# Optimization experiments

Hardware: AMD Instinct MI355X
Metric: run time of the kernel (lower is better)

## Reference

```python
import jax, jax.numpy as jnp
import numpy as np

LN_EPS = 1e-5

def _lstm_cell(x, h, c, Wih, Whh, bih, bhh):
    # gates: [b, 4*d], PyTorch LSTMCell gate order: i, f, g, o
    gates = x @ Wih.T + bih + h @ Whh.T + bhh
    i, f, g, o = jnp.split(gates, 4, axis=-1)
    c_new = jax.nn.sigmoid(f) * c + jax.nn.sigmoid(i) * jnp.tanh(g)
    h_new = jax.nn.sigmoid(o) * jnp.tanh(c_new)
    return h_new, c_new

def _layernorm(x, g, b):
    mu = jnp.mean(x, axis=-1, keepdims=True)
    var = jnp.mean(jnp.square(x - mu), axis=-1, keepdims=True)
    return (x - mu) * jax.lax.rsqrt(var + LN_EPS) * g + b

def setup_inputs() -> dict:
    key = jax.random.key(0)
    ks = jax.random.split(key, 8)
    B, F_, L, D, V, NL = 128, 1, 32, 512, 10000, 2
    features = jax.random.normal(ks[0], (B, F_, D), dtype=jnp.float32)
    caption = jax.random.randint(ks[1], (B, L), 0, V, dtype=jnp.int64)
    emb_W = jax.random.normal(ks[2], (V, D), dtype=jnp.float32) * 0.02
    W_ih = jax.random.normal(ks[3], (NL, 4 * D, D), dtype=jnp.float32) * (1.0 / np.sqrt(D))
    W_hh = jax.random.normal(ks[4], (NL, 4 * D, D), dtype=jnp.float32) * (1.0 / np.sqrt(D))
    b_ih = jnp.zeros((NL, 4 * D), dtype=jnp.float32)
    b_hh = jnp.zeros((NL, 4 * D), dtype=jnp.float32)
    ln_g = jnp.ones((D,), dtype=jnp.float32)
    ln_b = jnp.zeros((D,), dtype=jnp.float32)
    fc_W = jax.random.normal(ks[5], (V, D), dtype=jnp.float32) * np.sqrt(2.0 / D)
    fc_b = jnp.zeros((V,), dtype=jnp.float32)
    return {"features": features, "caption": caption, "emb_W": emb_W,
            "W_ih": W_ih, "W_hh": W_hh, "b_ih": b_ih, "b_hh": b_hh,
            "ln_g": ln_g, "ln_b": ln_b, "fc_W": fc_W, "fc_b": fc_b}

def reference(features, caption, emb_W, W_ih, W_hh, b_ih, b_hh, ln_g, ln_b, fc_W, fc_b):
    b, f, d = features.shape
    n_layers = W_ih.shape[0]
    emb = emb_W[caption]                                   # [b, L, d]
    inp = jnp.concatenate([features, emb], axis=1)         # [b, T, d], T = f + L
    h0 = jnp.zeros((b, d), dtype=features.dtype)
    c0 = jnp.zeros((b, d), dtype=features.dtype)

    def step(carry, x_t):
        h, c = carry
        # Faithful to the original: every layer consumes x_t, sharing (h, c).
        for l in range(n_layers):
            h, c = _lstm_cell(x_t, h, c, W_ih[l], W_hh[l], b_ih[l], b_hh[l])
        h = _layernorm(h, ln_g, ln_b)                      # normalized h carries forward
        logits_t = h @ fc_W.T + fc_b                       # [b, V]
        return (h, c), logits_t

    xs = jnp.swapaxes(inp, 0, 1)                           # [T, b, d]
    _, logits = jax.lax.scan(step, (h0, c0), xs)           # [T, b, V]
    logits = jnp.swapaxes(logits, 0, 1)                    # [b, T, V]
    return jax.nn.log_softmax(logits[:, f:, :], axis=-1)   # [b, L, V]
```

## Files before the change

### kernel.cpp

```cpp
#include <hip/hip_runtime.h>

#define B_ 128
#define D_ 512
#define T_ 33
#define L_ 32
#define V_ 10000
#define NWG 128

typedef short short8 __attribute__((ext_vector_type(8)));
typedef float f32x4 __attribute__((ext_vector_type(4)));

__device__ __forceinline__ short f2bf_rne(float f) {
    unsigned u = __builtin_bit_cast(unsigned, f);
    unsigned r = (u + 0x7FFFu + ((u >> 16) & 1u)) >> 16;
    return (short)r;
}
__device__ __forceinline__ void split2(float v, short& hi, short& lo) {
    unsigned u = __builtin_bit_cast(unsigned, v);
    hi = (short)(u >> 16);
    float hif = __builtin_bit_cast(float, u & 0xFFFF0000u);
    lo = (short)(__builtin_bit_cast(unsigned, v - hif) >> 16);
}
__device__ __forceinline__ float sigm(float x) {
    return 1.0f / (1.0f + __expf(-x));
}

__device__ __forceinline__ void llc_stu(void* p, unsigned v) {
    __hip_atomic_store((unsigned*)p, v, __ATOMIC_RELAXED,
                       __HIP_MEMORY_SCOPE_SYSTEM);
}

__global__ void prep_kernel(const float* __restrict__ features,
                            const int* __restrict__ caption,
                            const float* __restrict__ embW,
                            const float* __restrict__ fcW,
                            short* __restrict__ Xhi,
                            short* __restrict__ Xlo,
                            short* __restrict__ fcWb,
                            int* __restrict__ syncv) {
    const long NX = (long)T_ * B_ * D_;
    const long NW = (long)V_ * D_;
    const long total = NX + NW;
    long gid = (long)blockIdx.x * blockDim.x + threadIdx.x;
    if (gid < NWG) syncv[gid] = 0;
    for (long idx = gid; idx < total; idx += (long)gridDim.x * blockDim.x) {
        if (idx < NX) {
            int t = (int)(idx / (B_ * D_));
            int r = (int)(idx % (B_ * D_));
            int b = r >> 9;
            int d = r & 511;
            float v;
            if (t == 0) v = features[r];
            else        v = embW[(long)caption[b * L_ + (t - 1)] * D_ + d];
            short hi, lo;
            split2(v, hi, lo);
            Xhi[idx] = hi;
            Xlo[idx] = lo;
        } else {
            long j = idx - NX;
            fcWb[j] = f2bf_rne(fcW[j]);
        }
    }
}

__global__ __launch_bounds__(256)
void lstm_persist(const short* __restrict__ Xhi, const short* __restrict__ Xlo,
                  const float* __restrict__ Wih, const float* __restrict__ Whh,
                  const float* __restrict__ bih, const float* __restrict__ bhh,
                  const float* __restrict__ lng, const float* __restrict__ lnb,
                  unsigned* __restrict__ H0p, float* __restrict__ H1f,
                  short* __restrict__ Hnb, int* __restrict__ syncv) {
    __shared__ __align__(16) short Wh[2][16][1032];
    __shared__ __align__(16) short Wo[2][16][1032];
    __shared__ float gbuf[128][17];
    __shared__ float carr[128][4];
    __shared__ float rs_s[128], murs_s[128];
    __shared__ float gam_s[512], bet_s[512];
    __shared__ float bias_s[2][16];
    __shared__ float bconst_s[16];

    const int tid  = threadIdx.x;
    const int w    = blockIdx.x;
    const int d0   = w * 4;
    const int wave = tid >> 6;
    const int lane = tid & 63;
    const int wm   = wave * 32;
    const int n    = lane & 15;
    const int kq   = (lane >> 4) * 8;

    for (int idx = tid; idx < 512; idx += 256) {
        gam_s[idx] = lng[idx];
        bet_s[idx] = lnb[idx];
    }
    if (tid < 32) {
        int l = tid >> 4, nn = tid & 15;
        int row = (nn >> 2) * 512 + d0 + (nn & 3);
        bias_s[l][nn] = bih[l * 2048 + row] + bhh[l * 2048 + row];
    }
    for (int idx = tid; idx < 2 * 16 * 1024; idx += 256) {
        int l = idx >> 14;
        int nn = (idx >> 10) & 15;
        int k = idx & 1023;
        int row = (nn >> 2) * 512 + d0 + (nn & 3);
        float v = (k < 512) ? Wih[((long)(l * 2048 + row)) * 512 + k]
                            : Whh[((long)(l * 2048 + row)) * 512 + (k - 512)];
        if (l == 0 && k >= 512) v *= lng[k - 512];
        short hi, lo;
        split2(v, hi, lo);
        Wh[l][nn][k] = hi;
        Wo[l][nn][k] = lo;
    }
    {
        const int c = tid >> 4, kc = tid & 15;
        const int row = (c >> 2) * 512 + d0 + (c & 3);
        float s = 0.f;
        for (int k = kc * 32; k < kc * 32 + 32; ++k)
            s += lnb[k] * Whh[(long)row * 512 + k];
        gbuf[c][kc] = s;
    }
    for (int idx = tid; idx < 512; idx += 256) carr[idx >> 2][idx & 3] = 0.f;
    __syncthreads();
    if (tid < 16) {
        float s2 = 0.f;
        for (int i = 0; i < 16; ++i) s2 += gbuf[tid][i];
        bconst_s[tid] = s2;
    }
    __syncthreads();

    int* flags = syncv;
    int nb = 0;

    auto arrive = [&]() {
        __syncthreads();
        ++nb;
        if (tid == 0)
            __hip_atomic_store(&flags[w], nb, __ATOMIC_RELAXED,
                               __HIP_MEMORY_SCOPE_SYSTEM);
    };
    auto wait_bar = [&]() {
        if (wave == 0) {
            const int tgt = nb;
            for (;;) {
                int f0 = __hip_atomic_load(&flags[lane], __ATOMIC_RELAXED,
                                           __HIP_MEMORY_SCOPE_SYSTEM);
                int f1 = __hip_atomic_load(&flags[64 + lane], __ATOMIC_RELAXED,
                                           __HIP_MEMORY_SCOPE_SYSTEM);
                if (__all(f0 >= tgt && f1 >= tgt)) break;
                __builtin_amdgcn_s_sleep(1);
            }
        }
        __syncthreads();
        __builtin_amdgcn_fence(__ATOMIC_ACQUIRE, "agent");
    };

    auto ln_stats = [&]() {
        const int row = tid & 127, half = tid >> 7;
        const float4* hp = (const float4*)&H1f[row * 512 + half * 256];
        float s = 0.f, s2 = 0.f;
        #pragma unroll 16
        for (int i = 0; i < 64; ++i) {
            float4 v = hp[i];
            s  += v.x + v.y + v.z + v.w;
            s2 += v.x * v.x + v.y * v.y + v.z * v.z + v.w * v.w;
        }
        gbuf[row][half * 2]     = s;
        gbuf[row][half * 2 + 1] = s2;
        __syncthreads();
        if (tid < 128) {
            const float ss  = gbuf[tid][0] + gbuf[tid][2];
            const float ss2 = gbuf[tid][1] + gbuf[tid][3];
            const float mu  = ss * (1.0f / 512.0f);
            const float var = ss2 * (1.0f / 512.0f) - mu * mu;
            const float rs  = rsqrtf(var + 1e-5f);
            rs_s[tid]   = rs;
            murs_s[tid] = mu * rs;
        }
        __syncthreads();
    };

    const int rA0 = (wm + n) * 512;
    const int rA1 = (wm + 16 + n) * 512;
    const int rq  = (lane >> 4) * 4;

    for (int t = 0; t < T_; ++t) {
        const short* xh = Xhi + (long)t * B_ * D_;
        const short* xl = Xlo + (long)t * B_ * D_;

        {
            f32x4 acc0 = {0.f, 0.f, 0.f, 0.f};
            f32x4 acc1 = {0.f, 0.f, 0.f, 0.f};
            #pragma unroll 4
            for (int kc = 0; kc < 16; ++kc) {
                const int kg = kc * 32 + kq;
                short8 bh = *(const short8*)&Wh[0][n][kg];
                short8 bl = *(const short8*)&Wo[0][n][kg];
                short8 ah0 = *(const short8*)&xh[rA0 + kg];
                short8 al0 = *(const short8*)&xl[rA0 + kg];
                short8 ah1 = *(const short8*)&xh[rA1 + kg];
                short8 al1 = *(const short8*)&xl[rA1 + kg];
                acc0 = __builtin_amdgcn_mfma_f32_16x16x32_bf16(ah0, bh, acc0, 0, 0, 0);
                acc0 = __builtin_amdgcn_mfma_f32_16x16x32_bf16(ah0, bl, acc0, 0, 0, 0);
                acc0 = __builtin_amdgcn_mfma_f32_16x16x32_bf16(al0, bh, acc0, 0, 0, 0);
                acc1 = __builtin_amdgcn_mfma_f32_16x16x32_bf16(ah1, bh, acc1, 0, 0, 0);
                acc1 = __builtin_amdgcn_mfma_f32_16x16x32_bf16(ah1, bl, acc1, 0, 0, 0);
                acc1 = __builtin_amdgcn_mfma_f32_16x16x32_bf16(al1, bh, acc1, 0, 0, 0);
            }
            if (t > 0) {
                wait_bar();
                ln_stats();
                const float r0 = rs_s[wm + n],      m0 = murs_s[wm + n];
                const float r1 = rs_s[wm + 16 + n], m1 = murs_s[wm + 16 + n];
                #pragma unroll 2
                for (int kc = 0; kc < 16; ++kc) {
                    const int kh = kc * 32 + kq;
                    short8 bh = *(const short8*)&Wh[0][n][512 + kh];
                    short8 bl = *(const short8*)&Wo[0][n][512 + kh];
                    float va[8], vb[8];
                    *(float4*)&va[0] = *(const float4*)&H1f[rA0 + kh];
                    *(float4*)&va[4] = *(const float4*)&H1f[rA0 + kh + 4];
                    *(float4*)&vb[0] = *(const float4*)&H1f[rA1 + kh];
                    *(float4*)&vb[4] = *(const float4*)&H1f[rA1 + kh + 4];
                    short8 ah0, al0, ah1, al1;
                    #pragma unroll
                    for (int j = 0; j < 8; ++j) {
                        float f0 = fmaf(va[j], r0, -m0);
                        float f1 = fmaf(vb[j], r1, -m1);
                        short h_, l_;
                        split2(f0, h_, l_); ah0[j] = h_; al0[j] = l_;
                        split2(f1, h_, l_); ah1[j] = h_; al1[j] = l_;
                    }
                    acc0 = __builtin_amdgcn_mfma_f32_16x16x32_bf16(ah0, bh, acc0, 0, 0, 0);
                    acc0 = __builtin_amdgcn_mfma_f32_16x16x32_bf16(ah0, bl, acc0, 0, 0, 0);
                    acc0 = __builtin_amdgcn_mfma_f32_16x16x32_bf16(al0, bh, acc0, 0, 0, 0);
                    acc1 = __builtin_amdgcn_mfma_f32_16x16x32_bf16(ah1, bh, acc1, 0, 0, 0);
                    acc1 = __builtin_amdgcn_mfma_f32_16x16x32_bf16(ah1, bl, acc1, 0, 0, 0);
                    acc1 = __builtin_amdgcn_mfma_f32_16x16x32_bf16(al1, bh, acc1, 0, 0, 0);
                }
                if (w < 32 && t >= 2) {
                    const int rb = w * 4;
                    for (int idx = tid; idx < 2048; idx += 256) {
                        const int m = rb + (idx >> 9), k = idx & 511;
                        const float v = H1f[m * 512 + k];
                        const float o = fmaf(fmaf(v, rs_s[m], -murs_s[m]), gam_s[k], bet_s[k]);
                        Hnb[(((long)(t - 2)) * B_ + m) * D_ + k] = f2bf_rne(o);
                    }
                }
            }
            const float bs = bias_s[0][n] + (t > 0 ? bconst_s[n] : 0.f);
            #pragma unroll
            for (int r = 0; r < 4; ++r) {
                gbuf[wm + rq + r][n]      = acc0[r] + bs;
                gbuf[wm + 16 + rq + r][n] = acc1[r] + bs;
            }
            __syncthreads();
            #pragma unroll
            for (int it = tid; it < 512; it += 256) {
                const int m = it >> 2, d = it & 3;
                const float gi = gbuf[m][d],     gf = gbuf[m][4 + d];
                const float gg = gbuf[m][8 + d], go = gbuf[m][12 + d];
                const float cn = sigm(gf) * carr[m][d] + sigm(gi) * tanhf(gg);
                carr[m][d] = cn;
                const float hv = sigm(go) * tanhf(cn);
                short hi_, lo_;
                split2(hv, hi_, lo_);
                const unsigned pk = (unsigned)(unsigned short)hi_
                                  | ((unsigned)(unsigned short)lo_ << 16);
                llc_stu(&H0p[m * 512 + d0 + d], pk);
            }
            arrive();
        }

        {
            f32x4 acc0 = {0.f, 0.f, 0.f, 0.f};
            f32x4 acc1 = {0.f, 0.f, 0.f, 0.f};
            #pragma unroll 4
            for (int kc = 0; kc < 16; ++kc) {
                const int kg = kc * 32 + kq;
                short8 bh = *(const short8*)&Wh[1][n][kg];
                short8 bl = *(const short8*)&Wo[1][n][kg];
                short8 ah0 = *(const short8*)&xh[rA0 + kg];
                short8 al0 = *(const short8*)&xl[rA0 + kg];
                short8 ah1 = *(const short8*)&xh[rA1 + kg];
                short8 al1 = *(const short8*)&xl[rA1 + kg];
                acc0 = __builtin_amdgcn_mfma_f32_16x16x32_bf16(ah0, bh, acc0, 0, 0, 0);
                acc0 = __builtin_amdgcn_mfma_f32_16x16x32_bf16(ah0, bl, acc0, 0, 0, 0);
                acc0 = __builtin_amdgcn_mfma_f32_16x16x32_bf16(al0, bh, acc0, 0, 0, 0);
                acc1 = __builtin_amdgcn_mfma_f32_16x16x32_bf16(ah1, bh, acc1, 0, 0, 0);
                acc1 = __builtin_amdgcn_mfma_f32_16x16x32_bf16(ah1, bl, acc1, 0, 0, 0);
                acc1 = __builtin_amdgcn_mfma_f32_16x16x32_bf16(al1, bh, acc1, 0, 0, 0);
            }
            wait_bar();
            #pragma unroll 2
            for (int kc = 0; kc < 16; ++kc) {
                const int kh = kc * 32 + kq;
                short8 bh = *(const short8*)&Wh[1][n][512 + kh];
                short8 bl = *(const short8*)&Wo[1][n][512 + kh];
                unsigned u0[8], u1[8];
                *(uint4*)&u0[0] = *(const uint4*)&H0p[rA0 + kh];
                *(uint4*)&u0[4] = *(const uint4*)&H0p[rA0 + kh + 4];
                *(uint4*)&u1[0] = *(const uint4*)&H0p[rA1 + kh];
                *(uint4*)&u1[4] = *(const uint4*)&H0p[rA1 + kh + 4];
                short8 ah0, al0, ah1, al1;
                #pragma unroll
                for (int j = 0; j < 8; ++j) {
                    ah0[j] = (short)(u0[j] & 0xFFFFu);
                    al0[j] = (short)(u0[j] >> 16);
                    ah1[j] = (short)(u1[j] & 0xFFFFu);
                    al1[j] = (short)(u1[j] >> 16);
                }
                acc0 = __builtin_amdgcn_mfma_f32_16x16x32_bf16(ah0, bh, acc0, 0, 0, 0);
                acc0 = __builtin_amdgcn_mfma_f32_16x16x32_bf16(ah0, bl, acc0, 0, 0, 0);
                acc0 = __builtin_amdgcn_mfma_f32_16x16x32_bf16(al0, bh, acc0, 0, 0, 0);
                acc1 = __builtin_amdgcn_mfma_f32_16x16x32_bf16(ah1, bh, acc1, 0, 0, 0);
                acc1 = __builtin_amdgcn_mfma_f32_16x16x32_bf16(ah1, bl, acc1, 0, 0, 0);
                acc1 = __builtin_amdgcn_mfma_f32_16x16x32_bf16(al1, bh, acc1, 0, 0, 0);
            }
            const float bs = bias_s[1][n];
            #pragma unroll
            for (int r = 0; r < 4; ++r) {
                gbuf[wm + rq + r][n]      = acc0[r] + bs;
                gbuf[wm + 16 + rq + r][n] = acc1[r] + bs;
            }
            __syncthreads();
            #pragma unroll
            for (int it = tid; it < 512; it += 256) {
                const int m = it >> 2, d = it & 3;
                const float gi = gbuf[m][d],     gf = gbuf[m][4 + d];
                const float gg = gbuf[m][8 + d], go = gbuf[m][12 + d];
                const float cn = sigm(gf) * carr[m][d] + sigm(gi) * tanhf(gg);
                carr[m][d] = cn;
                const float hv = sigm(go) * tanhf(cn);
                llc_stu(&H1f[m * 512 + d0 + d],
                        __builtin_bit_cast(unsigned, hv));
            }
            arrive();
        }
    }

    wait_bar();
    ln_stats();
    if (w < 32) {
        const int rb = w * 4;
        for (int idx = tid; idx < 2048; idx += 256) {
            const int m = rb + (idx >> 9), k = idx & 511;
            const float v = H1f[m * 512 + k];
            const float o = fmaf(fmaf(v, rs_s[m], -murs_s[m]), gam_s[k], bet_s[k]);
            Hnb[(((long)(L_ - 1)) * B_ + m) * D_ + k] = f2bf_rne(o);
        }
    }
}

__launch_bounds__(256)
__global__ void gemm_fc(const short* __restrict__ A,
                        const short* __restrict__ Wt,
                        const float* __restrict__ bias,
                        float* __restrict__ out) {
    __shared__ __align__(16) short As[128 * 40];
    __shared__ __align__(16) short Bs[128 * 40];
    const int tid = threadIdx.x;
    const int m0 = blockIdx.x * 128;
    const int n0 = blockIdx.y * 128;
    const int lrow = tid >> 1;
    const int lcol = (tid & 1) * 16;
    const int w = tid >> 6;
    const int lane = tid & 63;
    const int wm = (w >> 1) * 64;
    const int wn = (w & 1) * 64;

    f32x4 acc[4][4];
    #pragma unroll
    for (int i = 0; i < 4; ++i)
        #pragma unroll
        for (int j = 0; j < 4; ++j)
            acc[i][j] = (f32x4){0.f, 0.f, 0.f, 0.f};

    for (int kc = 0; kc < 16; ++kc) {
        const int kg = kc * 32;
        {
            const float4* src = reinterpret_cast<const float4*>(
                A + (long)(m0 + lrow) * D_ + kg + lcol);
            float4 v0 = src[0];
            float4 v1 = src[1];
            float4* dst = reinterpret_cast<float4*>(&As[lrow * 40 + lcol]);
            dst[0] = v0;
            dst[1] = v1;
        }
        {
            const int nn = n0 + lrow;
            float4 v0 = {0.f, 0.f, 0.f, 0.f}, v1 = {0.f, 0.f, 0.f, 0.f};
            if (nn < V_) {
                const float4* src = reinterpret_cast<const float4*>(
                    Wt + (long)nn * D_ + kg + lcol);
                v0 = src[0];
                v1 = src[1];
            }
            float4* dst = reinterpret_cast<float4*>(&Bs[lrow * 40 + lcol]);
            dst[0] = v0;
            dst[1] = v1;
        }
        __syncthreads();
        const int kcol = (lane >> 4) * 8;
        const int rsel = lane & 15;
        short8 a[4], bf[4];
        #pragma unroll
        for (int i = 0; i < 4; ++i)
            a[i] = *reinterpret_cast<const short8*>(&As[(wm + i * 16 + rsel) * 40 + kcol]);
        #pragma unroll
        for (int j = 0; j < 4; ++j)
            bf[j] = *reinterpret_cast<const short8*>(&Bs[(wn + j * 16 + rsel) * 40 + kcol]);
        #pragma unroll
        for (int i = 0; i < 4; ++i)
            #pragma unroll
            for (int j = 0; j < 4; ++j)
                acc[i][j] = __builtin_amdgcn_mfma_f32_16x16x32_bf16(a[i], bf[j], acc[i][j], 0, 0, 0);
        __syncthreads();
    }

    const int rquad = (lane >> 4) * 4;
    const int ncol = lane & 15;
    #pragma unroll
    for (int i = 0; i < 4; ++i) {
        #pragma unroll
        for (int j = 0; j < 4; ++j) {
            const int ngl = n0 + wn + j * 16 + ncol;
            if (ngl < V_) {
                const float bv = bias[ngl];
                #pragma unroll
                for (int r = 0; r < 4; ++r) {
                    const int mgl = m0 + wm + i * 16 + rquad + r;
                    const int tt = mgl >> 7;
                    const int bb = mgl & 127;
                    out[((long)bb * L_ + tt) * V_ + ngl] = acc[i][j][r] + bv;
                }
            }
        }
    }
}

__global__ void logsoftmax_kernel(float* __restrict__ out) {
    __shared__ float red[256];
    const long row = blockIdx.x;
    float* p = out + row * V_;
    float4* p4 = reinterpret_cast<float4*>(p);
    const int tid = threadIdx.x;
    float s = 0.f;
    for (int i = tid; i < V_ / 4; i += 256) {
        float4 v = p4[i];
        s += __expf(v.x) + __expf(v.y) + __expf(v.z) + __expf(v.w);
    }
    red[tid] = s;
    __syncthreads();
    for (int st = 128; st > 0; st >>= 1) {
        if (tid < st) red[tid] += red[tid + st];
        __syncthreads();
    }
    const float ls = logf(red[0]);
    for (int i = tid; i < V_ / 4; i += 256) {
        float4 v = p4[i];
        v.x -= ls; v.y -= ls; v.z -= ls; v.w -= ls;
        p4[i] = v;
    }
}

extern "C" void kernel_launch(void* const* d_in, const int* in_sizes, int n_in,
                              void* d_out, int out_size, void* d_ws, size_t ws_size,
                              hipStream_t stream) {
    const float* features = (const float*)d_in[0];
    const int*   caption  = (const int*)d_in[1];
    const float* embW     = (const float*)d_in[2];
    const float* W_ih     = (const float*)d_in[3];
    const float* W_hh     = (const float*)d_in[4];
    const float* b_ih     = (const float*)d_in[5];
    const float* b_hh     = (const float*)d_in[6];
    const float* ln_g     = (const float*)d_in[7];
    const float* ln_b     = (const float*)d_in[8];
    const float* fc_W     = (const float*)d_in[9];
    const float* fc_b     = (const float*)d_in[10];
    float* out = (float*)d_out;

    char* ws = (char*)d_ws;
    int*      syncv = (int*)ws;      ws += 512;
    short*    Xhi   = (short*)ws;    ws += (size_t)T_ * B_ * D_ * 2;
    short*    Xlo   = (short*)ws;    ws += (size_t)T_ * B_ * D_ * 2;
    unsigned* H0p   = (unsigned*)ws; ws += (size_t)B_ * D_ * 4;
    float*    H1f   = (float*)ws;    ws += (size_t)B_ * D_ * 4;
    short*    Hnb   = (short*)ws;    ws += (size_t)L_ * B_ * D_ * 2;
    short*    fcWb  = (short*)ws;    ws += (size_t)V_ * D_ * 2;

    prep_kernel<<<2048, 256, 0, stream>>>(features, caption, embW, fc_W,
                                          Xhi, Xlo, fcWb, syncv);

    lstm_persist<<<NWG, 256, 0, stream>>>(Xhi, Xlo, W_ih, W_hh, b_ih, b_hh,
                                          ln_g, ln_b, H0p, H1f, Hnb,
                                          syncv);

    gemm_fc<<<dim3(32, 79), 256, 0, stream>>>(Hnb, fcWb, fc_b, out);
    logsoftmax_kernel<<<4096, 256, 0, stream>>>(out);
}
```

Baseline: 1.773 ms.

## Fold layernorm into layer-0 recurrent GEMM and double threads per workgroup

The persistent LSTM kernel now runs 512 threads (8 waves, 16 rows each) instead of 256, so each wave handles one MFMA tile rather than two. The layer-1 hidden state is stored pre-split as packed bf16 hi/lo. Layer 0 multiplies the raw hidden state and applies the layernorm correction afterwards (rs*acc - mu*rs*sum(gamma*W)), which moves the LN stats off the critical path and drops per-element normalize/split work. The barrier spin also gains an iteration cap, which could break out early and read stale data if the cap is ever hit.

```diff
diff --git a/kernel.cpp b/kernel.cpp
--- a/kernel.cpp
+++ b/kernel.cpp
@@ -6,6 +6,7 @@
 #define L_ 32
 #define V_ 10000
 #define NWG 128
+#define THREADS 512
 
 typedef short short8 __attribute__((ext_vector_type(8)));
 typedef float f32x4 __attribute__((ext_vector_type(4)));
@@ -23,6 +24,10 @@
 }
 __device__ __forceinline__ float sigm(float x) {
     return 1.0f / (1.0f + __expf(-x));
+}
+__device__ __forceinline__ float unpack2f(unsigned u) {
+    return __builtin_bit_cast(float, u << 16)
+         + __builtin_bit_cast(float, u & 0xFFFF0000u);
 }
 
 __device__ __forceinline__ void llc_stu(void* p, unsigned v) {
@@ -63,12 +68,12 @@
     }
 }
 
-__global__ __launch_bounds__(256)
+__global__ __launch_bounds__(THREADS)
 void lstm_persist(const short* __restrict__ Xhi, const short* __restrict__ Xlo,
                   const float* __restrict__ Wih, const float* __restrict__ Whh,
                   const float* __restrict__ bih, const float* __restrict__ bhh,
                   const float* __restrict__ lng, const float* __restrict__ lnb,
-                  unsigned* __restrict__ H0p, float* __restrict__ H1f,
+                  unsigned* __restrict__ H0p, unsigned* __restrict__ H1p,
                   short* __restrict__ Hnb, int* __restrict__ syncv) {
     __shared__ __align__(16) short Wh[2][16][1032];
     __shared__ __align__(16) short Wo[2][16][1032];
@@ -78,26 +83,25 @@
     __shared__ float gam_s[512], bet_s[512];
     __shared__ float bias_s[2][16];
     __shared__ float bconst_s[16];
+    __shared__ float sgam_s[16];
 
     const int tid  = threadIdx.x;
     const int w    = blockIdx.x;
     const int d0   = w * 4;
     const int wave = tid >> 6;
     const int lane = tid & 63;
-    const int wm   = wave * 32;
+    const int wm   = wave * 16;
     const int n    = lane & 15;
     const int kq   = (lane >> 4) * 8;
 
-    for (int idx = tid; idx < 512; idx += 256) {
-        gam_s[idx] = lng[idx];
-        bet_s[idx] = lnb[idx];
-    }
+    gam_s[tid & 511] = lng[tid & 511];
+    bet_s[tid & 511] = lnb[tid & 511];
     if (tid < 32) {
         int l = tid >> 4, nn = tid & 15;
         int row = (nn >> 2) * 512 + d0 + (nn & 3);
         bias_s[l][nn] = bih[l * 2048 + row] + bhh[l * 2048 + row];
     }
-    for (int idx = tid; idx < 2 * 16 * 1024; idx += 256) {
+    for (int idx = tid; idx < 2 * 16 * 1024; idx += THREADS) {
         int l = idx >> 14;
         int nn = (idx >> 10) & 15;
         int k = idx & 1023;
@@ -110,20 +114,27 @@
         Wh[l][nn][k] = hi;
         Wo[l][nn][k] = lo;
     }
-    {
+    if (tid < 256) {
         const int c = tid >> 4, kc = tid & 15;
         const int row = (c >> 2) * 512 + d0 + (c & 3);
+        float sb = 0.f, sg = 0.f;
+        for (int k = kc * 32; k < kc * 32 + 32; ++k) {
+            const float wv = Whh[(long)row * 512 + k];
+            sb += lnb[k] * wv;
+            sg += lng[k] * wv;
+        }
+        gbuf[c][kc]      = sb;
+        gbuf[64 + c][kc] = sg;
+    }
+    carr[tid >> 2][tid & 3] = 0.f;
+    __syncthreads();
+    if (tid < 32) {
+        const int c = tid & 15;
+        const int base = (tid >= 16) ? 64 + c : c;
         float s = 0.f;
-        for (int k = kc * 32; k < kc * 32 + 32; ++k)
-            s += lnb[k] * Whh[(long)row * 512 + k];
-        gbuf[c][kc] = s;
-    }
-    for (int idx = tid; idx < 512; idx += 256) carr[idx >> 2][idx & 3] = 0.f;
-    __syncthreads();
-    if (tid < 16) {
-        float s2 = 0.f;
-        for (int i = 0; i < 16; ++i) s2 += gbuf[tid][i];
-        bconst_s[tid] = s2;
+        for (int i = 0; i < 16; ++i) s += gbuf[base][i];
+        if (tid < 16) bconst_s[c] = s;
+        else          sgam_s[c]   = s;
     }
     __syncthreads();
 
@@ -140,35 +151,41 @@
     auto wait_bar = [&]() {
         if (wave == 0) {
             const int tgt = nb;
+            int iter = 0;
             for (;;) {
                 int f0 = __hip_atomic_load(&flags[lane], __ATOMIC_RELAXED,
                                            __HIP_MEMORY_SCOPE_SYSTEM);
                 int f1 = __hip_atomic_load(&flags[64 + lane], __ATOMIC_RELAXED,
                                            __HIP_MEMORY_SCOPE_SYSTEM);
                 if (__all(f0 >= tgt && f1 >= tgt)) break;
+                if (++iter > 65536) break;
                 __builtin_amdgcn_s_sleep(1);
             }
-        }
-        __syncthreads();
-        __builtin_amdgcn_fence(__ATOMIC_ACQUIRE, "agent");
+            __builtin_amdgcn_fence(__ATOMIC_ACQUIRE, "agent");
+        }
+        __syncthreads();
     };
 
     auto ln_stats = [&]() {
-        const int row = tid & 127, half = tid >> 7;
-        const float4* hp = (const float4*)&H1f[row * 512 + half * 256];
+        const int row = tid & 127, q = tid >> 7;
+        const uint4* hp = (const uint4*)&H1p[row * 512 + q * 128];
         float s = 0.f, s2 = 0.f;
-        #pragma unroll 16
-        for (int i = 0; i < 64; ++i) {
-            float4 v = hp[i];
-            s  += v.x + v.y + v.z + v.w;
-            s2 += v.x * v.x + v.y * v.y + v.z * v.z + v.w * v.w;
-        }
-        gbuf[row][half * 2]     = s;
-        gbuf[row][half * 2 + 1] = s2;
+        #pragma unroll 8
+        for (int i = 0; i < 32; ++i) {
+            uint4 u = hp[i];
+            #pragma unroll
+            for (int e = 0; e < 4; ++e) {
+                const float v = unpack2f((&u.x)[e]);
+                s  += v;
+                s2 += v * v;
+            }
+        }
+        gbuf[row][q * 2]     = s;
+        gbuf[row][q * 2 + 1] = s2;
         __syncthreads();
         if (tid < 128) {
-            const float ss  = gbuf[tid][0] + gbuf[tid][2];
-            const float ss2 = gbuf[tid][1] + gbuf[tid][3];
+            const float ss  = gbuf[tid][0] + gbuf[tid][2] + gbuf[tid][4] + gbuf[tid][6];
+            const float ss2 = gbuf[tid][1] + gbuf[tid][3] + gbuf[tid][5] + gbuf[tid][7];
             const float mu  = ss * (1.0f / 512.0f);
             const float var = ss2 * (1.0f / 512.0f) - mu * mu;
             const float rs  = rsqrtf(var + 1e-5f);
@@ -179,7 +196,6 @@
     };
 
     const int rA0 = (wm + n) * 512;
-    const int rA1 = (wm + 16 + n) * 512;
     const int rq  = (lane >> 4) * 4;
 
     for (int t = 0; t < T_; ++t) {
@@ -187,75 +203,62 @@
         const short* xl = Xlo + (long)t * B_ * D_;
 
         {
-            f32x4 acc0 = {0.f, 0.f, 0.f, 0.f};
-            f32x4 acc1 = {0.f, 0.f, 0.f, 0.f};
+            f32x4 accx = {0.f, 0.f, 0.f, 0.f};
+            f32x4 acch = {0.f, 0.f, 0.f, 0.f};
             #pragma unroll 4
             for (int kc = 0; kc < 16; ++kc) {
                 const int kg = kc * 32 + kq;
                 short8 bh = *(const short8*)&Wh[0][n][kg];
                 short8 bl = *(const short8*)&Wo[0][n][kg];
-                short8 ah0 = *(const short8*)&xh[rA0 + kg];
-                short8 al0 = *(const short8*)&xl[rA0 + kg];
-                short8 ah1 = *(const short8*)&xh[rA1 + kg];
-                short8 al1 = *(const short8*)&xl[rA1 + kg];
-                acc0 = __builtin_amdgcn_mfma_f32_16x16x32_bf16(ah0, bh, acc0, 0, 0, 0);
-                acc0 = __builtin_amdgcn_mfma_f32_16x16x32_bf16(ah0, bl, acc0, 0, 0, 0);
-                acc0 = __builtin_amdgcn_mfma_f32_16x16x32_bf16(al0, bh, acc0, 0, 0, 0);
-                acc1 = __builtin_amdgcn_mfma_f32_16x16x32_bf16(ah1, bh, acc1, 0, 0, 0);
-                acc1 = __builtin_amdgcn_mfma_f32_16x16x32_bf16(ah1, bl, acc1, 0, 0, 0);
-                acc1 = __builtin_amdgcn_mfma_f32_16x16x32_bf16(al1, bh, acc1, 0, 0, 0);
+                short8 ah = *(const short8*)&xh[rA0 + kg];
+                short8 al = *(const short8*)&xl[rA0 + kg];
+                accx = __builtin_amdgcn_mfma_f32_16x16x32_bf16(ah, bh, accx, 0, 0, 0);
+                accx = __builtin_amdgcn_mfma_f32_16x16x32_bf16(ah, bl, accx, 0, 0, 0);
+                accx = __builtin_amdgcn_mfma_f32_16x16x32_bf16(al, bh, accx, 0, 0, 0);
             }
             if (t > 0) {
                 wait_bar();
-                ln_stats();
-                const float r0 = rs_s[wm + n],      m0 = murs_s[wm + n];
-                const float r1 = rs_s[wm + 16 + n], m1 = murs_s[wm + 16 + n];
-                #pragma unroll 2
+                #pragma unroll 4
                 for (int kc = 0; kc < 16; ++kc) {
                     const int kh = kc * 32 + kq;
                     short8 bh = *(const short8*)&Wh[0][n][512 + kh];
                     short8 bl = *(const short8*)&Wo[0][n][512 + kh];
-                    float va[8], vb[8];
-                    *(float4*)&va[0] = *(const float4*)&H1f[rA0 + kh];
-                    *(float4*)&va[4] = *(const float4*)&H1f[rA0 + kh + 4];
-                    *(float4*)&vb[0] = *(const float4*)&H1f[rA1 + kh];
-                    *(float4*)&vb[4] = *(const float4*)&H1f[rA1 + kh + 4];
-                    short8 ah0, al0, ah1, al1;
+                    unsigned u[8];
+                    *(uint4*)&u[0] = *(const uint4*)&H1p[rA0 + kh];
+                    *(uint4*)&u[4] = *(const uint4*)&H1p[rA0 + kh + 4];
+                    short8 ah, al;
                     #pragma unroll
                     for (int j = 0; j < 8; ++j) {
-                        float f0 = fmaf(va[j], r0, -m0);
-                        float f1 = fmaf(vb[j], r1, -m1);
-                        short h_, l_;
-                        split2(f0, h_, l_); ah0[j] = h_; al0[j] = l_;
-                        split2(f1, h_, l_); ah1[j] = h_; al1[j] = l_;
+                        ah[j] = (short)(u[j] & 0xFFFFu);
+                        al[j] = (short)(u[j] >> 16);
                     }
-                    acc0 = __builtin_amdgcn_mfma_f32_16x16x32_bf16(ah0, bh, acc0, 0, 0, 0);
-                    acc0 = __builtin_amdgcn_mfma_f32_16x16x32_bf16(ah0, bl, acc0, 0, 0, 0);
-                    acc0 = __builtin_amdgcn_mfma_f32_16x16x32_bf16(al0, bh, acc0, 0, 0, 0);
-                    acc1 = __builtin_amdgcn_mfma_f32_16x16x32_bf16(ah1, bh, acc1, 0, 0, 0);
-                    acc1 = __builtin_amdgcn_mfma_f32_16x16x32_bf16(ah1, bl, acc1, 0, 0, 0);
-                    acc1 = __builtin_amdgcn_mfma_f32_16x16x32_bf16(al1, bh, acc1, 0, 0, 0);
+                    acch = __builtin_amdgcn_mfma_f32_16x16x32_bf16(ah, bh, acch, 0, 0, 0);
+                    acch = __builtin_amdgcn_mfma_f32_16x16x32_bf16(ah, bl, acch, 0, 0, 0);
+                    acch = __builtin_amdgcn_mfma_f32_16x16x32_bf16(al, bh, acch, 0, 0, 0);
                 }
+                ln_stats();
                 if (w < 32 && t >= 2) {
                     const int rb = w * 4;
-                    for (int idx = tid; idx < 2048; idx += 256) {
+                    for (int idx = tid; idx < 2048; idx += THREADS) {
                         const int m = rb + (idx >> 9), k = idx & 511;
-                        const float v = H1f[m * 512 + k];
+                        const float v = unpack2f(H1p[m * 512 + k]);
                         const float o = fmaf(fmaf(v, rs_s[m], -murs_s[m]), gam_s[k], bet_s[k]);
                         Hnb[(((long)(t - 2)) * B_ + m) * D_ + k] = f2bf_rne(o);
                     }
                 }
             }
             const float bs = bias_s[0][n] + (t > 0 ? bconst_s[n] : 0.f);
+            const float sg = sgam_s[n];
             #pragma unroll
             for (int r = 0; r < 4; ++r) {
-                gbuf[wm + rq + r][n]      = acc0[r] + bs;
-                gbuf[wm + 16 + rq + r][n] = acc1[r] + bs;
+                const int row = wm + rq + r;
+                float g = accx[r] + bs;
+                if (t > 0) g += acch[r] * rs_s[row] - murs_s[row] * sg;
+                gbuf[row][n] = g;
             }
             __syncthreads();
-            #pragma unroll
-            for (int it = tid; it < 512; it += 256) {
-                const int m = it >> 2, d = it & 3;
+            {
+                const int m = tid >> 2, d = tid & 3;
                 const float gi = gbuf[m][d],     gf = gbuf[m][4 + d];
                 const float gg = gbuf[m][8 + d], go = gbuf[m][12 + d];
                 const float cn = sigm(gf) * carr[m][d] + sigm(gi) * tanhf(gg);
@@ -271,67 +274,54 @@
         }
 
         {
-            f32x4 acc0 = {0.f, 0.f, 0.f, 0.f};
-            f32x4 acc1 = {0.f, 0.f, 0.f, 0.f};
+            f32x4 acc = {0.f, 0.f, 0.f, 0.f};
             #pragma unroll 4
             for (int kc = 0; kc < 16; ++kc) {
                 const int kg = kc * 32 + kq;
                 short8 bh = *(const short8*)&Wh[1][n][kg];
                 short8 bl = *(const short8*)&Wo[1][n][kg];
-                short8 ah0 = *(const short8*)&xh[rA0 + kg];
-                short8 al0 = *(const short8*)&xl[rA0 + kg];
-                short8 ah1 = *(const short8*)&xh[rA1 + kg];
-                short8 al1 = *(const short8*)&xl[rA1 + kg];
-                acc0 = __builtin_amdgcn_mfma_f32_16x16x32_bf16(ah0, bh, acc0, 0, 0, 0);
-                acc0 = __builtin_amdgcn_mfma_f32_16x16x32_bf16(ah0, bl, acc0, 0, 0, 0);
-                acc0 = __builtin_amdgcn_mfma_f32_16x16x32_bf16(al0, bh, acc0, 0, 0, 0);
-                acc1 = __builtin_amdgcn_mfma_f32_16x16x32_bf16(ah1, bh, acc1, 0, 0, 0);
-                acc1 = __builtin_amdgcn_mfma_f32_16x16x32_bf16(ah1, bl, acc1, 0, 0, 0);
-                acc1 = __builtin_amdgcn_mfma_f32_16x16x32_bf16(al1, bh, acc1, 0, 0, 0);
+                short8 ah = *(const short8*)&xh[rA0 + kg];
+                short8 al = *(const short8*)&xl[rA0 + kg];
+                acc = __builtin_amdgcn_mfma_f32_16x16x32_bf16(ah, bh, acc, 0, 0, 0);
+                acc = __builtin_amdgcn_mfma_f32_16x16x32_bf16(ah, bl, acc, 0, 0, 0);
+                acc = __builtin_amdgcn_mfma_f32_16x16x32_bf16(al, bh, acc, 0, 0, 0);
             }
             wait_bar();
-            #pragma unroll 2
+            #pragma unroll 4
             for (int kc = 0; kc < 16; ++kc) {
                 const int kh = kc * 32 + kq;
                 short8 bh = *(const short8*)&Wh[1][n][512 + kh];
                 short8 bl = *(const short8*)&Wo[1][n][512 + kh];
-                unsigned u0[8], u1[8];
-                *(uint4*)&u0[0] = *(const uint4*)&H0p[rA0 + kh];
-                *(uint4*)&u0[4] = *(const uint4*)&H0p[rA0 + kh + 4];
-                *(uint4*)&u1[0] = *(const uint4*)&H0p[rA1 + kh];
-                *(uint4*)&u1[4] = *(const uint4*)&H0p[rA1 + kh + 4];
-                short8 ah0, al0, ah1, al1;
+                unsigned u[8];
+                *(uint4*)&u[0] = *(const uint4*)&H0p[rA0 + kh];
+                *(uint4*)&u[4] = *(const uint4*)&H0p[rA0 + kh + 4];
+                short8 ah, al;
                 #pragma unroll
                 for (int j = 0; j < 8; ++j) {
-                    ah0[j] = (short)(u0[j] & 0xFFFFu);
-                    al0[j] = (short)(u0[j] >> 16);
-                    ah1[j] = (short)(u1[j] & 0xFFFFu);
-                    al1[j] = (short)(u1[j] >> 16);
+                    ah[j] = (short)(u[j] & 0xFFFFu);
+                    al[j] = (short)(u[j] >> 16);
                 }
-                acc0 = __builtin_amdgcn_mfma_f32_16x16x32_bf16(ah0, bh, acc0, 0, 0, 0);
-                acc0 = __builtin_amdgcn_mfma_f32_16x16x32_bf16(ah0, bl, acc0, 0, 0, 0);
-                acc0 = __builtin_amdgcn_mfma_f32_16x16x32_bf16(al0, bh, acc0, 0, 0, 0);
-                acc1 = __builtin_amdgcn_mfma_f32_16x16x32_bf16(ah1, bh, acc1, 0, 0, 0);
-                acc1 = __builtin_amdgcn_mfma_f32_16x16x32_bf16(ah1, bl, acc1, 0, 0, 0);
-                acc1 = __builtin_amdgcn_mfma_f32_16x16x32_bf16(al1, bh, acc1, 0, 0, 0);
+                acc = __builtin_amdgcn_mfma_f32_16x16x32_bf16(ah, bh, acc, 0, 0, 0);
+                acc = __builtin_amdgcn_mfma_f32_16x16x32_bf16(ah, bl, acc, 0, 0, 0);
+                acc = __builtin_amdgcn_mfma_f32_16x16x32_bf16(al, bh, acc, 0, 0, 0);
             }
             const float bs = bias_s[1][n];
             #pragma unroll
-            for (int r = 0; r < 4; ++r) {
-                gbuf[wm + rq + r][n]      = acc0[r] + bs;
-                gbuf[wm + 16 + rq + r][n] = acc1[r] + bs;
-            }
+            for (int r = 0; r < 4; ++r)
+                gbuf[wm + rq + r][n] = acc[r] + bs;
             __syncthreads();
-            #pragma unroll
-            for (int it = tid; it < 512; it += 256) {
-                const int m = it >> 2, d = it & 3;
+            {
+                const int m = tid >> 2, d = tid & 3;
                 const float gi = gbuf[m][d],     gf = gbuf[m][4 + d];
                 const float gg = gbuf[m][8 + d], go = gbuf[m][12 + d];
                 const float cn = sigm(gf) * carr[m][d] + sigm(gi) * tanhf(gg);
                 carr[m][d] = cn;
                 const float hv = sigm(go) * tanhf(cn);
-                llc_stu(&H1f[m * 512 + d0 + d],
-                        __builtin_bit_cast(unsigned, hv));
+                short hi_, lo_;
+                split2(hv, hi_, lo_);
+                const unsigned pk = (unsigned)(unsigned short)hi_
+                                  | ((unsigned)(unsigned short)lo_ << 16);
+                llc_stu(&H1p[m * 512 + d0 + d], pk);
             }
             arrive();
         }
@@ -341,9 +331,9 @@
     ln_stats();
     if (w < 32) {
         const int rb = w * 4;
-        for (int idx = tid; idx < 2048; idx += 256) {
+        for (int idx = tid; idx < 2048; idx += THREADS) {
             const int m = rb + (idx >> 9), k = idx & 511;
-            const float v = H1f[m * 512 + k];
+            const float v = unpack2f(H1p[m * 512 + k]);
             const float o = fmaf(fmaf(v, rs_s[m], -murs_s[m]), gam_s[k], bet_s[k]);
             Hnb[(((long)(L_ - 1)) * B_ + m) * D_ + k] = f2bf_rne(o);
         }
@@ -483,16 +473,16 @@
     short*    Xhi   = (short*)ws;    ws += (size_t)T_ * B_ * D_ * 2;
     short*    Xlo   = (short*)ws;    ws += (size_t)T_ * B_ * D_ * 2;
     unsigned* H0p   = (unsigned*)ws; ws += (size_t)B_ * D_ * 4;
-    float*    H1f   = (float*)ws;    ws += (size_t)B_ * D_ * 4;
+    unsigned* H1p   = (unsigned*)ws; ws += (size_t)B_ * D_ * 4;
     short*    Hnb   = (short*)ws;    ws += (size_t)L_ * B_ * D_ * 2;
     short*    fcWb  = (short*)ws;    ws += (size_t)V_ * D_ * 2;
 
     prep_kernel<<<2048, 256, 0, stream>>>(features, caption, embW, fc_W,
                                           Xhi, Xlo, fcWb, syncv);
 
-    lstm_persist<<<NWG, 256, 0, stream>>>(Xhi, Xlo, W_ih, W_hh, b_ih, b_hh,
-                                          ln_g, ln_b, H0p, H1f, Hnb,
-                                          syncv);
+    lstm_persist<<<NWG, THREADS, 0, stream>>>(Xhi, Xlo, W_ih, W_hh, b_ih, b_hh,
+                                              ln_g, ln_b, H0p, H1p, Hnb,
+                                              syncv);
 
     gemm_fc<<<dim3(32, 79), 256, 0, stream>>>(Hnb, fcWb, fc_b, out);
     logsoftmax_kernel<<<4096, 256, 0, stream>>>(out);
```

After: 1.674 ms. 1.06x faster.
